# Optimization experiments

Hardware: AMD Instinct MI355X
Metric: run time of the kernel (lower is better)

## Reference

```python
import jax, jax.numpy as jnp
import numpy as np

N_HEAD = 16
ROPE_THETA = 10000.0


def setup_inputs() -> dict:
    key = jax.random.key(0)
    k0, k1, k2 = jax.random.split(key, 3)
    B, T, C = 2, 2048, 1024
    s = 0.02  # GPT-2 style init scale
    return {
        "x": jax.random.normal(k0, (B, T, C), jnp.float32),
        "w_attn": jax.random.normal(k1, (C, 3 * C), jnp.float32) * s,
        "b_attn": jnp.zeros((3 * C,), jnp.float32),
        "w_proj": jax.random.normal(k2, (C, C), jnp.float32) * s,
        "b_proj": jnp.zeros((C,), jnp.float32),
    }


def _rope(x):
    # x: [B, H, T, D]; interleaved-pair rotary (lucidrains rotate_queries_or_keys)
    T, D = x.shape[-2], x.shape[-1]
    inv_freq = 1.0 / (ROPE_THETA ** (jnp.arange(0, D, 2, dtype=jnp.float32) / D))
    freqs = jnp.arange(T, dtype=jnp.float32)[:, None] * inv_freq[None, :]  # [T, D/2]
    emb = jnp.repeat(freqs, 2, axis=-1)  # [T, D], each freq duplicated per pair
    cos, sin = jnp.cos(emb), jnp.sin(emb)
    xr = x.reshape(*x.shape[:-1], D // 2, 2)
    x1, x2 = xr[..., 0], xr[..., 1]
    rot = jnp.stack((-x2, x1), axis=-1).reshape(x.shape)  # rotate_half
    return x * cos + rot * sin


def reference(x, w_attn, b_attn, w_proj, b_proj):
    B, T, C = x.shape
    H = N_HEAD
    D = C // H
    qkv = x @ w_attn + b_attn                      # [B, T, 3C]
    q, k, v = jnp.split(qkv, 3, axis=-1)

    def heads(t):
        return t.reshape(B, T, H, D).transpose(0, 2, 1, 3)  # [B, H, T, D]

    q, k, v = heads(q), heads(k), heads(v)
    q = _rope(q)
    k = _rope(k)

    att = jnp.einsum("bhqd,bhkd->bhqk", q, k) * (1.0 / np.sqrt(D))
    causal = jnp.tril(jnp.ones((T, T), dtype=bool))
    att = jnp.where(causal, att, -jnp.inf)
    att = jax.nn.softmax(att, axis=-1)
    y = jnp.einsum("bhqk,bhkd->bhqd", att, v)
    y = y.transpose(0, 2, 1, 3).reshape(B, T, C)
    return y @ w_proj + b_proj
```

## Files before the change

kernel.cpp:

```cpp
#include <hip/hip_runtime.h>
#include <hip/hip_bf16.h>
#include <stdint.h>

typedef __hip_bfloat16 bf16;
typedef __attribute__((ext_vector_type(8))) short bf16x8;
typedef __attribute__((ext_vector_type(4))) short bf16x4;
typedef __attribute__((ext_vector_type(4))) float f32x4;

__device__ inline float bf2f(bf16 v) { return __bfloat162float(v); }
__device__ inline bf16 f2bf(float f) { return __float2bfloat16(f); }

__device__ inline void glds16(const void* g, void* l) {
    __builtin_amdgcn_global_load_lds(
        (const __attribute__((address_space(1))) uint32_t*)g,
        (__attribute__((address_space(3))) uint32_t*)l, 16, 0, 0);
}

__device__ inline void conv_wt_tile(const float* __restrict__ W,
                                    bf16* __restrict__ Wt, int N, int K,
                                    int bx, int by, int tid, bf16 (*t)[72])
{
    const int n0 = bx * 64, k0 = by * 64;
#pragma unroll
    for (int p = 0; p < 4; ++p) {
        int idx = p * 256 + tid;
        int kr = idx >> 4, c4 = idx & 15;
        float4 f = *(const float4*)(W + (size_t)(k0 + kr) * N + n0 + c4 * 4);
        t[kr][c4 * 4 + 0] = f2bf(f.x); t[kr][c4 * 4 + 1] = f2bf(f.y);
        t[kr][c4 * 4 + 2] = f2bf(f.z); t[kr][c4 * 4 + 3] = f2bf(f.w);
    }
    __syncthreads();
#pragma unroll
    for (int p = 0; p < 2; ++p) {
        int idx = p * 256 + tid;
        int nr = idx >> 3, ch = idx & 7;
        union { bf16x8 v; bf16 e[8]; } u;
#pragma unroll
        for (int j = 0; j < 8; ++j) u.e[j] = t[ch * 8 + j][nr];
        *(bf16x8*)(Wt + (size_t)(n0 + nr) * K + k0 + ch * 8) = u.v;
    }
}

__global__ __launch_bounds__(256) void prep(
    const float* __restrict__ x, bf16* __restrict__ xbf,
    const float* __restrict__ w_attn, bf16* __restrict__ wat,
    const float* __restrict__ w_proj, bf16* __restrict__ wpt,
    float2* __restrict__ tab)
{
    __shared__ bf16 t[64][72];
    const int bid = blockIdx.x;
    const int tid = threadIdx.x;
    if (bid < 2048) {
        size_t i = ((size_t)bid * 256 + tid) * 8;
        float4 f0 = *(const float4*)(x + i);
        float4 f1 = *(const float4*)(x + i + 4);
        union { bf16x8 v; bf16 e[8]; } u;
        u.e[0] = f2bf(f0.x); u.e[1] = f2bf(f0.y); u.e[2] = f2bf(f0.z); u.e[3] = f2bf(f0.w);
        u.e[4] = f2bf(f1.x); u.e[5] = f2bf(f1.y); u.e[6] = f2bf(f1.z); u.e[7] = f2bf(f1.w);
        *(bf16x8*)(xbf + i) = u.v;
    } else if (bid < 2816) {
        int idx = bid - 2048;
        conv_wt_tile(w_attn, wat, 3072, 1024, idx % 48, idx / 48, tid, t);
    } else if (bid < 3072) {
        int idx = bid - 2816;
        conv_wt_tile(w_proj, wpt, 1024, 1024, idx % 16, idx / 16, tid, t);
    } else {
        int gid = (bid - 3072) * 256 + tid;
        int p = gid & 31, tt = gid >> 5;
        float invf = expf(-(float)(2 * p) * (9.210340371976184f / 64.0f));
        float sn, cs;
        sincosf((float)tt * invf, &sn, &cs);
        tab[gid] = make_float2(cs, sn);
    }
}

__global__ __launch_bounds__(256) void gemm_qkv(
    const bf16* __restrict__ A, const bf16* __restrict__ Bt,
    const float* __restrict__ bias, const float2* __restrict__ tab,
    bf16* __restrict__ qh, bf16* __restrict__ kh, bf16* __restrict__ vt)
{
    const int K = 1024;
    __shared__ __align__(16) bf16 sa[128 * 64];
    __shared__ __align__(16) bf16 sb[128 * 64];

    const int tid  = threadIdx.x;
    const int wave = tid >> 6, lane = tid & 63;
    const int quad = lane >> 4, l16 = lane & 15;
    const int wm = wave >> 1, wn = wave & 1;
    const int row0 = blockIdx.x * 128, n0 = blockIdx.y * 128;

    f32x4 acc[4][4] = {};

    const int srow = lane >> 3;
    const int schk = lane & 7;

    for (int k0 = 0; k0 < K; k0 += 64) {
        __syncthreads();
#pragma unroll
        for (int half = 0; half < 2; ++half) {
#pragma unroll
            for (int g = 0; g < 2; ++g) {
                int rowb = half * 64 + wave * 16 + g * 8;
                int row  = rowb + srow;
                glds16(A + (size_t)(row0 + row) * K + k0 + ((schk ^ row) & 7) * 8,
                       &sa[rowb * 64]);
                glds16(Bt + (size_t)(n0 + row) * K + k0 + ((schk ^ row) & 7) * 8,
                       &sb[rowb * 64]);
            }
        }
        __syncthreads();

#pragma unroll
        for (int kk = 0; kk < 2; ++kk) {
            bf16x8 af[4], bfr[4];
#pragma unroll
            for (int mi = 0; mi < 4; ++mi) {
                int row = wm * 64 + mi * 16 + l16;
                af[mi] = *(const bf16x8*)&sa[row * 64 + (((kk * 4 + quad) ^ row) & 7) * 8];
            }
#pragma unroll
            for (int ni = 0; ni < 4; ++ni) {
                int row = wn * 64 + ni * 16 + l16;
                bfr[ni] = *(const bf16x8*)&sb[row * 64 + (((kk * 4 + quad) ^ row) & 7) * 8];
            }
#pragma unroll
            for (int mi = 0; mi < 4; ++mi)
#pragma unroll
                for (int ni = 0; ni < 4; ++ni)
                    acc[mi][ni] = __builtin_amdgcn_mfma_f32_16x16x32_bf16(
                        af[mi], bfr[ni], acc[mi][ni], 0, 0, 0);
        }
    }

    const float QS = 0.125f * 1.44269504088896f;
#pragma unroll
    for (int ni = 0; ni < 4; ++ni) {
        int col = n0 + wn * 64 + ni * 16 + l16;
        float bvv = bias[col];
        int sec = col >> 10;
        int cd  = col & 1023;
        int h   = cd >> 6, d = cd & 63;
        if (sec == 2) {
#pragma unroll
            for (int mi = 0; mi < 4; ++mi) {
                int trow = row0 + wm * 64 + mi * 16 + quad * 4;
                int tt0 = trow & 2047, bb = trow >> 11;
                union { bf16x4 v; bf16 e[4]; } pv;
#pragma unroll
                for (int r = 0; r < 4; ++r) pv.e[r] = f2bf(acc[mi][ni][r] + bvv);
                *(bf16x4*)(vt + ((size_t)((bb * 16 + h) * 64 + d)) * 2048 + tt0) = pv.v;
            }
        } else {
            int p   = d >> 1;
            bool odd = (d & 1) != 0;
#pragma unroll
            for (int mi = 0; mi < 4; ++mi) {
#pragma unroll
                for (int r = 0; r < 4; ++r) {
                    int row = row0 + wm * 64 + mi * 16 + quad * 4 + r;
                    float v = acc[mi][ni][r] + bvv;
                    float vp = __shfl_xor(v, 1);
                    int tt = row & 2047, b = row >> 11;
                    float2 cssn = tab[tt * 32 + p];
                    float ro = odd ? (v * cssn.x + vp * cssn.y)
                                   : (v * cssn.x - vp * cssn.y);
                    size_t dst = (((size_t)(b * 16 + h)) * 2048 + tt) * 64 + d;
                    if (sec == 0) qh[dst] = f2bf(ro * QS);
                    else          kh[dst] = f2bf(ro);
                }
            }
        }
    }
}

__global__ __launch_bounds__(256) void gemm_proj(
    const bf16* __restrict__ A, const bf16* __restrict__ Bt,
    const float* __restrict__ bias, float* __restrict__ out)
{
    const int N = 1024, K = 1024;
    __shared__ __align__(16) bf16 sa[64 * 64];
    __shared__ __align__(16) bf16 sb[64 * 64];

    const int tid  = threadIdx.x;
    const int wave = tid >> 6, lane = tid & 63;
    const int quad = lane >> 4, l16 = lane & 15;
    const int row0 = blockIdx.x * 64, n0 = blockIdx.y * 64;

    f32x4 acc[4] = {};

    const int srow = lane >> 3;
    const int schk = lane & 7;

    for (int k0 = 0; k0 < K; k0 += 64) {
        __syncthreads();
#pragma unroll
        for (int g = 0; g < 2; ++g) {
            int rowb = wave * 16 + g * 8;
            int row  = rowb + srow;
            glds16(A + (size_t)(row0 + row) * K + k0 + ((schk ^ row) & 7) * 8,
                   &sa[rowb * 64]);
        }
#pragma unroll
        for (int g = 0; g < 2; ++g) {
            int rowb = wave * 16 + g * 8;
            int row  = rowb + srow;
            glds16(Bt + (size_t)(n0 + row) * K + k0 + ((schk ^ row) & 7) * 8,
                   &sb[rowb * 64]);
        }
        __syncthreads();

#pragma unroll
        for (int kk = 0; kk < 2; ++kk) {
            bf16x8 af[4], bfr;
#pragma unroll
            for (int mi = 0; mi < 4; ++mi) {
                int row = mi * 16 + l16;
                af[mi] = *(const bf16x8*)&sa[row * 64 + (((kk * 4 + quad) ^ row) & 7) * 8];
            }
            {
                int row = wave * 16 + l16;
                bfr = *(const bf16x8*)&sb[row * 64 + (((kk * 4 + quad) ^ row) & 7) * 8];
            }
#pragma unroll
            for (int mi = 0; mi < 4; ++mi)
                acc[mi] = __builtin_amdgcn_mfma_f32_16x16x32_bf16(
                    af[mi], bfr, acc[mi], 0, 0, 0);
        }
    }

    {
        int col = n0 + wave * 16 + l16;
        float bvv = bias[col];
#pragma unroll
        for (int mi = 0; mi < 4; ++mi) {
#pragma unroll
            for (int r = 0; r < 4; ++r) {
                int row = row0 + mi * 16 + quad * 4 + r;
                out[(size_t)row * N + col] = acc[mi][r] + bvv;
            }
        }
    }
}

__global__ __launch_bounds__(256) void attn_k(
    const bf16* __restrict__ qg, const bf16* __restrict__ kg,
    const bf16* __restrict__ vtg, bf16* __restrict__ y)
{
    __shared__ __align__(16) bf16 sK[128 * 64];
    __shared__ __align__(16) bf16 sV[64 * 128];
    __shared__ __align__(16) bf16 pL[4][16][136];

    const int tid  = threadIdx.x;
    const int wave = tid >> 6, lane = tid & 63;
    const int quad = lane >> 4, l16 = lane & 15;
    const int bh   = blockIdx.x;
    const int qt   = 31 - (int)blockIdx.y;
    const bf16* Q  = qg  + (size_t)bh * 2048 * 64;
    const bf16* K  = kg  + (size_t)bh * 2048 * 64;
    const bf16* Vt = vtg + (size_t)bh * 64 * 2048;
    const int b = bh >> 4, h = bh & 15;

    const int q0 = qt * 64 + wave * 16;

    bf16x8 aq[2];
    aq[0] = *(const bf16x8*)(Q + (size_t)(q0 + l16) * 64 + quad * 8);
    aq[1] = *(const bf16x8*)(Q + (size_t)(q0 + l16) * 64 + 32 + quad * 8);

    const bf16* kptr[4];
    const bf16* vptr[4];
#pragma unroll
    for (int c = 0; c < 4; ++c) {
        int key = wave * 32 + c * 8 + (lane >> 3);
        int p   = lane & 7;
        kptr[c] = K + (size_t)key * 64 + ((p ^ key) & 7) * 8;
        int d   = wave * 16 + c * 4 + (lane >> 4);
        int pv  = lane & 15;
        vptr[c] = Vt + (size_t)d * 2048 + ((pv ^ d) & 15) * 8;
    }

    union { bf16x8 v; short e[8]; } uo;
#pragma unroll
    for (int j = 0; j < 8; ++j) uo.e[j] = (short)0x3F80;
    const bf16x8 vones = uo.v;

    f32x4 o[4] = {};
    f32x4 ls   = {};
    float m_r[4] = {-1e30f, -1e30f, -1e30f, -1e30f};
    const float THR = 8.0f;

    for (int kt = 0; kt <= q0 + 15; kt += 128) {
        __syncthreads();
#pragma unroll
        for (int c = 0; c < 4; ++c) {
            glds16(kptr[c], &sK[(wave * 32 + c * 8) * 64]);
            kptr[c] += 128 * 64;
        }
#pragma unroll
        for (int c = 0; c < 4; ++c) {
            glds16(vptr[c], &sV[(wave * 16 + c * 4) * 128]);
            vptr[c] += 128;
        }
        __syncthreads();

        const int nlast = min(7, (q0 - kt) >> 4);
        f32x4 sc[8];
        __builtin_amdgcn_s_setprio(1);
#pragma unroll
        for (int nt = 0; nt < 8; ++nt) {
            if (nt > nlast) continue;
            int key = nt * 16 + l16;
            f32x4 s0 = {};
            bf16x8 bk0 = *(const bf16x8*)&sK[key * 64 + ((quad ^ key) & 7) * 8];
            s0 = __builtin_amdgcn_mfma_f32_16x16x32_bf16(aq[0], bk0, s0, 0, 0, 0);
            bf16x8 bk1 = *(const bf16x8*)&sK[key * 64 + (((4 + quad) ^ key) & 7) * 8];
            sc[nt] = __builtin_amdgcn_mfma_f32_16x16x32_bf16(aq[1], bk1, s0, 0, 0, 0);
        }
        __builtin_amdgcn_s_setprio(0);
        {
            const int diag = (q0 - kt) >> 4;
            if (diag <= 7) {
                int key = kt + diag * 16 + l16;
#pragma unroll
                for (int r = 0; r < 4; ++r) {
                    int row = q0 + quad * 4 + r;
                    if (key > row) sc[diag][r] = -1e30f;
                }
            }
        }
        float rowmax[4] = {-1e30f, -1e30f, -1e30f, -1e30f};
#pragma unroll
        for (int nt = 0; nt < 8; ++nt) {
            if (nt > nlast) continue;
#pragma unroll
            for (int r = 0; r < 4; ++r) rowmax[r] = fmaxf(rowmax[r], sc[nt][r]);
        }
        bool okl = (rowmax[0] <= m_r[0] + THR) && (rowmax[1] <= m_r[1] + THR) &&
                   (rowmax[2] <= m_r[2] + THR) && (rowmax[3] <= m_r[3] + THR);
        if (!__all((int)okl)) {
#pragma unroll
            for (int off = 1; off < 16; off <<= 1)
#pragma unroll
                for (int r = 0; r < 4; ++r)
                    rowmax[r] = fmaxf(rowmax[r], __shfl_xor(rowmax[r], off));
            float alpha[4];
#pragma unroll
            for (int r = 0; r < 4; ++r) {
                float mn = fmaxf(m_r[r], rowmax[r]);
                alpha[r] = exp2f(m_r[r] - mn);
                m_r[r] = mn;
            }
#pragma unroll
            for (int nt = 0; nt < 4; ++nt)
#pragma unroll
                for (int r = 0; r < 4; ++r) o[nt][r] *= alpha[r];
#pragma unroll
            for (int r = 0; r < 4; ++r) ls[r] *= alpha[r];
        }
#pragma unroll
        for (int nt = 0; nt < 8; ++nt) {
            if (nt > nlast) continue;
#pragma unroll
            for (int r = 0; r < 4; ++r) sc[nt][r] = exp2f(sc[nt][r] - m_r[r]);
        }

#pragma unroll
        for (int nt = 0; nt < 8; ++nt) {
            if (nt > nlast) continue;
            int blk = (2 * nt + (l16 >> 3)) ^ quad;
#pragma unroll
            for (int r = 0; r < 4; ++r)
                pL[wave][quad * 4 + r][blk * 8 + (l16 & 7)] = f2bf(sc[nt][r]);
        }
        if (nlast < 7 && !(nlast & 1)) {
            int blk = (2 * (nlast + 1) + (l16 >> 3)) ^ quad;
#pragma unroll
            for (int r = 0; r < 4; ++r)
                pL[wave][quad * 4 + r][blk * 8 + (l16 & 7)] = f2bf(0.f);
        }
        __builtin_amdgcn_s_setprio(1);
#pragma unroll
        for (int c = 0; c < 4; ++c) {
            if (c > (nlast >> 1)) continue;
            bf16x8 pa = *(const bf16x8*)&pL[wave][l16][(((4 * c + quad) ^ (l16 >> 2)) * 8)];
            ls = __builtin_amdgcn_mfma_f32_16x16x32_bf16(pa, vones, ls, 0, 0, 0);
#pragma unroll
            for (int dnt = 0; dnt < 4; ++dnt) {
                int d = dnt * 16 + l16;
                int cc = c * 4 + quad;
                bf16x8 vb = *(const bf16x8*)&sV[d * 128 + ((cc ^ d) & 15) * 8];
                o[dnt] = __builtin_amdgcn_mfma_f32_16x16x32_bf16(pa, vb, o[dnt], 0, 0, 0);
            }
        }
        __builtin_amdgcn_s_setprio(0);
    }

#pragma unroll
    for (int r = 0; r < 4; ++r) {
        float inv = 1.0f / ls[r];
        int qq = q0 + quad * 4 + r;
#pragma unroll
        for (int nt = 0; nt < 4; ++nt) {
            int d = nt * 16 + l16;
            y[((size_t)(b * 2048 + qq)) * 1024 + h * 64 + d] = f2bf(o[nt][r] * inv);
        }
    }
}

extern "C" void kernel_launch(void* const* d_in, const int* in_sizes, int n_in,
                              void* d_out, int out_size, void* d_ws, size_t ws_size,
                              hipStream_t stream) {
    const float* x      = (const float*)d_in[0];
    const float* w_attn = (const float*)d_in[1];
    const float* b_attn = (const float*)d_in[2];
    const float* w_proj = (const float*)d_in[3];
    const float* b_proj = (const float*)d_in[4];
    float* out = (float*)d_out;

    bf16* xbf = (bf16*)d_ws;
    bf16* wat = xbf + (size_t)4194304;
    bf16* wpt = wat + (size_t)3145728;
    float2* tab = (float2*)(wpt + (size_t)1048576);
    bf16* qh  = wpt + (size_t)1048576 + 262144;
    bf16* kh  = qh  + (size_t)4194304;
    bf16* vt  = kh  + (size_t)4194304;
    bf16* yws = vt  + (size_t)4194304;

    dim3 blk(256);
    prep<<<dim3(3328), blk, 0, stream>>>(x, xbf, w_attn, wat, w_proj, wpt, tab);
    gemm_qkv<<<dim3(32, 24), blk, 0, stream>>>(xbf, wat, b_attn, tab, qh, kh, vt);
    attn_k<<<dim3(32, 32), blk, 0, stream>>>(qh, kh, vt, yws);
    gemm_proj<<<dim3(64, 16), blk, 0, stream>>>(yws, wpt, b_proj, out);
    (void)in_sizes; (void)n_in; (void)ws_size; (void)out_size;
}
```

Before: 210.1 us.

## Split KV range for long causal query tiles and add a combine kernel

For the 12 longest causal query tiles per head, the KV loop is split across two blocks. Each block writes unnormalised output plus its row max and row sum into workspace that reuses the no-longer-needed bf16 input buffer. A new combine kernel merges the two halves with log-sum-exp rescaling before the projection GEMM. A lookup table orders the 44 blocks per head to balance work across CUs, which should shorten the long causal tail. The cost is extra partial-result traffic and one more kernel launch.

```diff
diff --git a/kernel.cpp b/kernel.cpp
--- a/kernel.cpp
+++ b/kernel.cpp
@@ -242,9 +242,21 @@
     }
 }
 
+__device__ const signed char QT_TAB[44] = {
+    19,18,17,16, 31,31,30,30,28,29,15,14,
+    28,29,26,26,27,27,24,25,13,12,
+    24,25,22,22,23,23,20,21,11,10,
+    20,21, 9, 8, 7, 6, 5, 4, 3, 2, 1, 0};
+__device__ const signed char HALF_TAB[44] = {
+     2, 2, 2, 2,  0, 1, 0, 1, 0, 0, 2, 2,
+     1, 1, 0, 1, 0, 1, 0, 0, 2, 2,
+     1, 1, 0, 1, 0, 1, 0, 0, 2, 2,
+     1, 1, 2, 2, 2, 2, 2, 2, 2, 2, 2, 2};
+
 __global__ __launch_bounds__(256) void attn_k(
     const bf16* __restrict__ qg, const bf16* __restrict__ kg,
-    const bf16* __restrict__ vtg, bf16* __restrict__ y)
+    const bf16* __restrict__ vtg, bf16* __restrict__ y,
+    float* __restrict__ part)
 {
     __shared__ __align__(16) bf16 sK[128 * 64];
     __shared__ __align__(16) bf16 sV[64 * 128];
@@ -254,7 +266,15 @@
     const int wave = tid >> 6, lane = tid & 63;
     const int quad = lane >> 4, l16 = lane & 15;
     const int bh   = blockIdx.x;
-    const int qt   = 31 - (int)blockIdx.y;
+    const int yb   = (int)blockIdx.y;
+    const int qt   = QT_TAB[yb];
+    const int hv   = HALF_TAB[yb];
+    const bool split = (hv != 2);
+    const int ntiles = (qt >> 1) + 1;
+    const int nA     = (ntiles + 1) >> 1;
+    const int it0 = (split && hv == 1) ? nA : 0;
+    const int it1 = (split && hv == 0) ? nA : ntiles;
+
     const bf16* Q  = qg  + (size_t)bh * 2048 * 64;
     const bf16* K  = kg  + (size_t)bh * 2048 * 64;
     const bf16* Vt = vtg + (size_t)bh * 64 * 2048;
@@ -272,10 +292,10 @@
     for (int c = 0; c < 4; ++c) {
         int key = wave * 32 + c * 8 + (lane >> 3);
         int p   = lane & 7;
-        kptr[c] = K + (size_t)key * 64 + ((p ^ key) & 7) * 8;
+        kptr[c] = K + (size_t)key * 64 + ((p ^ key) & 7) * 8 + (size_t)it0 * (128 * 64);
         int d   = wave * 16 + c * 4 + (lane >> 4);
         int pv  = lane & 15;
-        vptr[c] = Vt + (size_t)d * 2048 + ((pv ^ d) & 15) * 8;
+        vptr[c] = Vt + (size_t)d * 2048 + ((pv ^ d) & 15) * 8 + it0 * 128;
     }
 
     union { bf16x8 v; short e[8]; } uo;
@@ -288,7 +308,8 @@
     float m_r[4] = {-1e30f, -1e30f, -1e30f, -1e30f};
     const float THR = 8.0f;
 
-    for (int kt = 0; kt <= q0 + 15; kt += 128) {
+    for (int it = it0; it < it1; ++it) {
+        const int kt = it << 7;
         __syncthreads();
 #pragma unroll
         for (int c = 0; c < 4; ++c) {
@@ -394,16 +415,62 @@
         __builtin_amdgcn_s_setprio(0);
     }
 
-#pragma unroll
-    for (int r = 0; r < 4; ++r) {
-        float inv = 1.0f / ls[r];
-        int qq = q0 + quad * 4 + r;
-#pragma unroll
-        for (int nt = 0; nt < 4; ++nt) {
-            int d = nt * 16 + l16;
-            y[((size_t)(b * 2048 + qq)) * 1024 + h * 64 + d] = f2bf(o[nt][r] * inv);
-        }
-    }
+    if (!split) {
+#pragma unroll
+        for (int r = 0; r < 4; ++r) {
+            float inv = 1.0f / ls[r];
+            int qq = q0 + quad * 4 + r;
+#pragma unroll
+            for (int nt = 0; nt < 4; ++nt) {
+                int d = nt * 16 + l16;
+                y[((size_t)(b * 2048 + qq)) * 1024 + h * 64 + d] = f2bf(o[nt][r] * inv);
+            }
+        }
+    } else {
+        float* pb = part + (size_t)((bh * 12 + (qt - 20)) * 2 + hv) * 4224;
+#pragma unroll
+        for (int r = 0; r < 4; ++r) {
+            int lrow = wave * 16 + quad * 4 + r;
+#pragma unroll
+            for (int nt = 0; nt < 4; ++nt)
+                pb[lrow * 64 + nt * 16 + l16] = o[nt][r];
+            if (l16 == 0) {
+                pb[4096 + lrow] = m_r[r];
+                pb[4160 + lrow] = ls[r];
+            }
+        }
+    }
+}
+
+__global__ __launch_bounds__(256) void attn_combine(
+    const float* __restrict__ part, bf16* __restrict__ y)
+{
+    const int bh = blockIdx.x, qi = blockIdx.y, qt = 20 + qi;
+    const int b = bh >> 4, h = bh & 15;
+    const int tid = threadIdx.x;
+    const int row = tid >> 2;
+    const int d0  = (tid & 3) * 16;
+    const float* pA = part + (size_t)((bh * 12 + qi) * 2) * 4224;
+    const float* pB = pA + 4224;
+    float mA = pA[4096 + row], mB = pB[4096 + row];
+    float lA = pA[4160 + row], lB = pB[4160 + row];
+    float m  = fmaxf(mA, mB);
+    float sA = exp2f(mA - m), sB = exp2f(mB - m);
+    float inv = 1.0f / (lA * sA + lB * sB);
+    size_t yo = ((size_t)(b * 2048 + qt * 64 + row)) * 1024 + h * 64;
+    union { bf16x8 v; bf16 e[8]; } u0, u1;
+#pragma unroll
+    for (int j = 0; j < 8; ++j) {
+        float vA = pA[row * 64 + d0 + j], vB = pB[row * 64 + d0 + j];
+        u0.e[j] = f2bf((vA * sA + vB * sB) * inv);
+    }
+#pragma unroll
+    for (int j = 0; j < 8; ++j) {
+        float vA = pA[row * 64 + d0 + 8 + j], vB = pB[row * 64 + d0 + 8 + j];
+        u1.e[j] = f2bf((vA * sA + vB * sB) * inv);
+    }
+    *(bf16x8*)(y + yo + d0)     = u0.v;
+    *(bf16x8*)(y + yo + d0 + 8) = u1.v;
 }
 
 extern "C" void kernel_launch(void* const* d_in, const int* in_sizes, int n_in,
@@ -424,11 +491,13 @@
     bf16* kh  = qh  + (size_t)4194304;
     bf16* vt  = kh  + (size_t)4194304;
     bf16* yws = vt  + (size_t)4194304;
+    float* part = (float*)d_ws;
 
     dim3 blk(256);
     prep<<<dim3(3328), blk, 0, stream>>>(x, xbf, w_attn, wat, w_proj, wpt, tab);
     gemm_qkv<<<dim3(32, 24), blk, 0, stream>>>(xbf, wat, b_attn, tab, qh, kh, vt);
-    attn_k<<<dim3(32, 32), blk, 0, stream>>>(qh, kh, vt, yws);
+    attn_k<<<dim3(32, 44), blk, 0, stream>>>(qh, kh, vt, yws, part);
+    attn_combine<<<dim3(32, 12), blk, 0, stream>>>(part, yws);
     gemm_proj<<<dim3(64, 16), blk, 0, stream>>>(yws, wpt, b_proj, out);
     (void)in_sizes; (void)n_in; (void)ws_size; (void)out_size;
 }
```

Result: slower. 222.0 us (+5.6%).
